# Kernel tuning notes

Hardware: AMD Instinct MI355X
Metric: run time of the kernel (lower is better)

## Reference

```python
import jax, jax.numpy as jnp
import numpy as np

J_THR = 0.5
E_THR = 0.5
STRIDE = 4.0
N_LAYERS = 3
NFEAT = 256
SCORER_HIDDEN = 128


def setup_inputs() -> dict:
    key = jax.random.key(0)
    ks = jax.random.split(key, 8)
    B, C, h, w = 4, NFEAT, 128, 128
    inp = {
        "j_logits": jax.random.normal(ks[0], (B, 1, h, w), dtype=jnp.float32),
        "offsets": jax.random.uniform(ks[1], (B, 2, h, w), dtype=jnp.float32),
        "node_feats_map": jax.random.normal(ks[2], (B, C, h, w), dtype=jnp.float32) * 0.1,
        "W_self": jax.random.normal(ks[3], (N_LAYERS, C, C), dtype=jnp.float32) / np.sqrt(C).astype(np.float32),
        "W_nbr": jax.random.normal(ks[4], (N_LAYERS, C, C), dtype=jnp.float32) / np.sqrt(C).astype(np.float32),
        "b_gnn": jnp.zeros((N_LAYERS, C), dtype=jnp.float32),
        "Ws1": jax.random.normal(ks[5], (2 * C, SCORER_HIDDEN), dtype=jnp.float32) / np.sqrt(2.0 * C).astype(np.float32),
        "bs1": jnp.zeros((SCORER_HIDDEN,), dtype=jnp.float32),
        "Ws2": jax.random.normal(ks[6], (SCORER_HIDDEN,), dtype=jnp.float32) / np.sqrt(SCORER_HIDDEN).astype(np.float32),
        "bs2": jnp.zeros((), dtype=jnp.float32),
        "max_nodes": 256,
    }
    return inp


def _complete_graph(n):
    # src repeats node i (n-1) times; dst enumerates all j != i, matching torch complete_graph
    src = np.repeat(np.arange(n), n - 1)
    grid = np.tile(np.arange(n), (n, 1))
    dst = grid[~np.eye(n, dtype=bool)]
    return jnp.asarray(src, dtype=jnp.int32), jnp.asarray(dst, dtype=jnp.int32)


def reference(j_logits, offsets, node_feats_map, W_self, W_nbr, b_gnn, Ws1, bs1, Ws2, bs2, max_nodes):
    B, _, h, w = j_logits.shape
    C = node_feats_map.shape[1]
    N = int(max_nodes)
    src, dst = _complete_graph(N)  # [E], E = N*(N-1)

    def per_image(jl, off, nmap):
        prob = jax.nn.sigmoid(jl[0].reshape(-1))            # [h*w]
        topv, topi = jax.lax.top_k(prob, N)                  # fixed-size stream compaction
        valid = topv > J_THR                                 # [N] mask replacing dynamic nonzero
        iy = topi // w
        ix = topi % w
        yo = off[0].reshape(-1)[topi]
        xo = off[1].reshape(-1)[topi]
        xs = (ix.astype(jnp.float32) + 0.5 + xo) * STRIDE
        ys = (iy.astype(jnp.float32) + 0.5 + yo) * STRIDE
        nodes = jnp.stack([xs, ys], axis=-1)                 # [N,2]
        x = nmap.reshape(C, -1)[:, topi].T * valid[:, None].astype(nmap.dtype)  # [N,C]
        ev = (valid[src] & valid[dst]).astype(x.dtype)       # [E] edge validity
        deg = jax.ops.segment_sum(ev, dst, num_segments=N)   # [N]
        inv_deg = jnp.where(deg > 0, 1.0 / jnp.maximum(deg, 1.0), 0.0)
        for l in range(W_self.shape[0]):
            msg = x[src] * ev[:, None]                       # gather + mask [E,C]
            agg = jax.ops.segment_sum(msg, dst, num_segments=N) * inv_deg[:, None]
            x = jax.nn.relu(x @ W_self[l] + agg @ W_nbr[l] + b_gnn[l]) * valid[:, None].astype(x.dtype)
        hcat = jnp.concatenate([x[src], x[dst]], axis=-1)    # [E,2C]
        hid = jax.nn.relu(hcat @ Ws1 + bs1)                  # [E,H]
        logits = hid @ Ws2 + bs2                             # [E]
        probs = jax.nn.sigmoid(logits)
        keep = (probs > E_THR) & (ev > 0)
        return nodes, x, logits, keep

    nodes, node_emb, edge_logits, keep = jax.vmap(per_image)(j_logits, offsets, node_feats_map)
    return nodes, node_emb, edge_logits, keep
```

## Files before the change

kernel.cpp:

```cpp
#include <hip/hip_runtime.h>

#define NPIX 16384
#define NN   256
#define CC   256
#define HH   128
#define EE   65280
#define BB   4
#define NG   32

typedef __attribute__((ext_vector_type(8))) short short8;
typedef __attribute__((ext_vector_type(4))) float f32x4;

__device__ __forceinline__ unsigned short f2bf(float f){
  unsigned b = __float_as_uint(f);
  return (unsigned short)((b + 0x7fffu + ((b >> 16) & 1u)) >> 16);
}
__device__ __forceinline__ float bf2f(unsigned short s){ return __uint_as_float(((unsigned)s) << 16); }
__device__ __forceinline__ float bf_lo(unsigned u){ return __uint_as_float(u << 16); }
__device__ __forceinline__ float bf_hi(unsigned u){ return __uint_as_float(u & 0xFFFF0000u); }

__global__ __launch_bounds__(1024) void k_topk(
    const float* __restrict__ jl, const float* __restrict__ off,
    int* __restrict__ topi, int* __restrict__ valid, float* __restrict__ inv_deg,
    float* __restrict__ out_nodes, float* __restrict__ Sbuf,
    const float* __restrict__ Wself, const float* __restrict__ Wnbr,
    const float* __restrict__ Ws1,
    unsigned short* __restrict__ wbfT, unsigned short* __restrict__ wuvT)
{
  __shared__ int hist[NG][257];
  __shared__ int histT[256];
  __shared__ unsigned long long s_sel[NN];
  __shared__ unsigned long long s_T;
  __shared__ int s_digit, s_krem, s_cnt, s_vcnt, s_break;
  __shared__ float tile[32][33];

  const int bid = blockIdx.x;
  const int tid = threadIdx.x;

  if (bid >= BB) {
    const int blk = bid - BB;
    const int m = blk >> 6;
    const int t = blk & 63;
    const int r  = tid >> 5;
    const int cl = tid & 31;
    if (m < 6) {
      const int tr = t >> 3, tc = t & 7;
      const float* src = (m < 3) ? (Wself + (size_t)m*65536) : (Wnbr + (size_t)(m-3)*65536);
      tile[r][cl] = src[(size_t)(tr*32 + r)*256 + tc*32 + cl];
      __syncthreads();
      wbfT[(size_t)m*65536 + (size_t)(tc*32 + r)*256 + tr*32 + cl] = f2bf(tile[cl][r]);
    } else {
      const int tr = t >> 2, tc = t & 3;
      tile[r][cl] = Ws1[(size_t)(tr*32 + r)*128 + tc*32 + cl];
      __syncthreads();
      int h  = tc*32 + r;
      int cgx = tr*32 + cl;
      int col = h + ((cgx >= 256) ? 128 : 0);
      wuvT[(size_t)col*256 + (cgx & 255)] = f2bf(tile[cl][r]);
    }
    return;
  }

  const int b = bid;
  const int grp = tid >> 5;
  if (tid == 0) { s_cnt = 0; s_vcnt = 0; }

  {
    int l = tid >> 8, c = tid & 255;
    Sbuf[l*BB*CC + b*CC + c] = 0.0f;
  }

  unsigned long long rk[16];
  const float* p = jl + (size_t)b * NPIX;
  #pragma unroll
  for (int r = 0; r < 16; ++r) {
    int i = tid + (r << 10);
    float x = p[i];
    float pr = 1.0f / (1.0f + expf(-x));
    unsigned bits = __float_as_uint(pr);
    rk[r] = ((unsigned long long)bits << 32) | (unsigned)(0xFFFFFFFFu - (unsigned)i);
  }

  unsigned long long prefix = 0;
  int k = NN;
  int shift = 56;
  int brk = 0;
  for (int pass = 0; pass < 8 && !brk; ++pass) {
    shift = 56 - 8 * pass;
    for (int i = tid; i < NG * 257; i += 1024) ((int*)hist)[i] = 0;
    __syncthreads();
    unsigned long long pmask = (pass == 0) ? 0ULL : (~0ULL << (shift + 8));
    #pragma unroll
    for (int r = 0; r < 16; ++r) {
      unsigned long long kk = rk[r];
      if ((kk & pmask) == prefix)
        atomicAdd(&hist[grp][(int)((kk >> shift) & 255)], 1);
    }
    __syncthreads();
    if (tid < 256) {
      int t = 0;
      #pragma unroll
      for (int g = 0; g < NG; ++g) t += hist[g][tid];
      histT[tid] = t;
    }
    __syncthreads();
    if (tid < 64) {
      int h0 = histT[4*tid + 0], h1 = histT[4*tid + 1];
      int h2 = histT[4*tid + 2], h3 = histT[4*tid + 3];
      int tot = h0 + h1 + h2 + h3;
      int suf = tot;
      #pragma unroll
      for (int d = 1; d < 64; d <<= 1) {
        int o = __shfl_down(suf, d);
        if (tid + d < 64) suf += o;
      }
      int above = suf - tot;
      int c3 = h3 + above;
      int c2 = c3 + h2;
      int c1 = c2 + h1;
      int c0 = c1 + h0;
      if      (c3 >= k && above < k) { s_digit = 4*tid+3; s_krem = k - above; s_break = (h3 == 1); }
      else if (c2 >= k && c3    < k) { s_digit = 4*tid+2; s_krem = k - c3;    s_break = (h2 == 1); }
      else if (c1 >= k && c2    < k) { s_digit = 4*tid+1; s_krem = k - c2;    s_break = (h1 == 1); }
      else if (c0 >= k && c1    < k) { s_digit = 4*tid+0; s_krem = k - c1;    s_break = (h0 == 1); }
    }
    __syncthreads();
    prefix |= ((unsigned long long)s_digit) << shift;
    k = s_krem;
    brk = s_break;
  }

  if (shift == 0) {
    if (tid == 0) s_T = prefix;
  } else {
    unsigned long long known_mask = ~0ULL << shift;
    #pragma unroll
    for (int r = 0; r < 16; ++r)
      if ((rk[r] & known_mask) == prefix) s_T = rk[r];
  }
  __syncthreads();
  unsigned long long T = s_T;

  #pragma unroll
  for (int r = 0; r < 16; ++r) {
    unsigned long long kk = rk[r];
    if (kk >= T) { int pos = atomicAdd(&s_cnt, 1); s_sel[pos] = kk; }
  }
  __syncthreads();

  int my_rank = -1, my_v = 0;
  if (tid < NN) {
    unsigned long long mine = s_sel[tid];
    int rank = 0;
    #pragma unroll 16
    for (int j = 0; j < NN; ++j) rank += (s_sel[j] > mine) ? 1 : 0;
    unsigned bits = (unsigned)(mine >> 32);
    int v = bits > 0x3F000000u ? 1 : 0;
    int idx = (int)(0xFFFFFFFFu - (unsigned)(mine & 0xFFFFFFFFull));
    if (v) atomicAdd(&s_vcnt, 1);
    topi[b*NN + rank] = idx;
    valid[b*NN + rank] = v;
    int iy = idx >> 7;
    int ix = idx & 127;
    float yo = off[((size_t)b*2 + 0) * NPIX + idx];
    float xo = off[((size_t)b*2 + 1) * NPIX + idx];
    out_nodes[(b*NN + rank)*2 + 0] = ((float)ix + 0.5f + xo) * 4.0f;
    out_nodes[(b*NN + rank)*2 + 1] = ((float)iy + 0.5f + yo) * 4.0f;
    my_rank = rank; my_v = v;
  }
  __syncthreads();
  if (tid < NN) {
    int V = s_vcnt;
    inv_deg[b*NN + my_rank] = (my_v && V >= 2) ? 1.0f / (float)(V - 1) : 0.0f;
  }
}

__global__ __launch_bounds__(256) void k_gather(
    const float* __restrict__ nmap, const int* __restrict__ topi,
    const int* __restrict__ valid, unsigned short* __restrict__ x, float* __restrict__ S0)
{
  __shared__ int s_pix[8], s_val[8];
  const int blk = blockIdx.x;
  const int b  = blk >> 5;
  const int n0 = (blk & 31) * 8;
  const int c = threadIdx.x;
  if (c < 8) { s_pix[c] = topi[b*NN + n0 + c]; s_val[c] = valid[b*NN + n0 + c]; }
  __syncthreads();
  const float* base = nmap + ((size_t)b*CC + c) * NPIX;
  float sum = 0.f;
  #pragma unroll
  for (int r = 0; r < 8; ++r) {
    float val = s_val[r] ? base[s_pix[r]] : 0.0f;
    unsigned short hb = f2bf(val);
    x[(size_t)(b*NN + n0 + r)*CC + c] = hb;
    sum += bf2f(hb);
  }
  if (sum != 0.0f) atomicAdd(&S0[b*CC + c], sum);
}

__global__ __launch_bounds__(256) void k_gnn(
    const unsigned short* __restrict__ x, const float* __restrict__ S,
    const float* __restrict__ inv_deg, const int* __restrict__ valid,
    const unsigned short* __restrict__ wT1, const unsigned short* __restrict__ wT2,
    const float* __restrict__ bias, unsigned short* __restrict__ xout,
    float* __restrict__ Snext,
    float* __restrict__ out_emb)
{
  __shared__ float sA1[16][33];
  __shared__ float sA2[16][33];
  __shared__ float sP2p[8][33];
  __shared__ float sP2[32];
  const int mt = blockIdx.x >> 3;
  const int cg = blockIdx.x & 7;
  const int row0 = mt * 16;
  const int b = row0 >> 8;
  const int tid = threadIdx.x;
  const int wave = tid >> 6;
  const int lane = tid & 63;

  {
    const int cl = tid >> 3;
    const int kw = tid & 7;
    const uint4*  w4 = (const uint4*)(wT2 + (size_t)(cg*32 + cl)*256 + kw*32);
    const float4* S4 = (const float4*)(S + b*CC + kw*32);
    float a = 0.f;
    #pragma unroll
    for (int i = 0; i < 4; ++i) {
      uint4 q = w4[i];
      float4 s0 = S4[2*i], s1 = S4[2*i + 1];
      a += s0.x*bf_lo(q.x) + s0.y*bf_hi(q.x) + s0.z*bf_lo(q.y) + s0.w*bf_hi(q.y);
      a += s1.x*bf_lo(q.z) + s1.y*bf_hi(q.z) + s1.z*bf_lo(q.w) + s1.w*bf_hi(q.w);
    }
    sP2p[kw][cl] = a;
  }
  __syncthreads();
  if (tid < 32) {
    float s = 0.f;
    #pragma unroll
    for (int g = 0; g < 8; ++g) s += sP2p[g][tid];
    sP2[tid] = s;
  }

  const unsigned short* wT = (wave < 2) ? wT1 : wT2;
  const int colbase = cg*32 + (wave & 1)*16;
  const int arow = row0 + (lane & 15);
  const int koff = (lane >> 4) * 8;

  const short8* aptr = (const short8*)(x + (size_t)arow*256 + koff);
  const short8* bptr = (const short8*)(wT + (size_t)(colbase + (lane & 15))*256 + koff);

  f32x4 acc = {0.f, 0.f, 0.f, 0.f};
  #pragma unroll
  for (int kk = 0; kk < 8; ++kk) {
    short8 af = aptr[kk*4];
    short8 bf = bptr[kk*4];
    acc = __builtin_amdgcn_mfma_f32_16x16x32_bf16(af, bf, acc, 0, 0, 0);
  }

  {
    float* dst = (wave < 2) ? &sA1[0][0] : &sA2[0][0];
    int ccol = (wave & 1)*16 + (lane & 15);
    #pragma unroll
    for (int r = 0; r < 4; ++r) {
      int crow = (lane >> 4)*4 + r;
      dst[crow*33 + ccol] = acc[r];
    }
  }
  __syncthreads();

  const int row = tid >> 4;
  const int cp2 = tid & 15;
  const int gr = row0 + row;
  const int c0 = cg*32 + 2*cp2;
  float inv = inv_deg[gr];
  int   va  = valid[gr];
  float a10 = sA1[row][2*cp2], a11 = sA1[row][2*cp2+1];
  float a20 = sA2[row][2*cp2], a21 = sA2[row][2*cp2+1];
  float p0 = sP2[2*cp2], p1 = sP2[2*cp2+1];
  float o0 = fmaxf(a10 + inv*(p0 - a20) + bias[c0],     0.f); o0 = va ? o0 : 0.f;
  float o1 = fmaxf(a11 + inv*(p1 - a21) + bias[c0 + 1], 0.f); o1 = va ? o1 : 0.f;

  unsigned short h0 = f2bf(o0), h1 = f2bf(o1);
  ((unsigned*)xout)[(size_t)gr*128 + (cg*16 + cp2)] = (unsigned)h0 | ((unsigned)h1 << 16);
  if (out_emb) {
    float2 v; v.x = o0; v.y = o1;
    *(float2*)&out_emb[(size_t)gr*CC + c0] = v;
  }
  if (Snext) {
    __syncthreads();
    sA1[row][2*cp2]   = bf2f(h0);
    sA1[row][2*cp2+1] = bf2f(h1);
    __syncthreads();
    if (tid < 32) {
      float s = 0.f;
      #pragma unroll
      for (int r = 0; r < 16; ++r) s += sA1[r][tid];
      if (s != 0.f) atomicAdd(&Snext[b*CC + cg*32 + tid], s);
    }
  }
}

__global__ __launch_bounds__(256) void k_uv(
    const unsigned short* __restrict__ x, const unsigned short* __restrict__ wuvT,
    const float* __restrict__ bs1,
    float* __restrict__ u, float* __restrict__ vt)
{
  const int mt = blockIdx.x >> 2;
  const int cg = blockIdx.x & 3;
  const int row0 = mt * 16;
  const int b = row0 >> 8;
  const int wave = threadIdx.x >> 6;
  const int lane = threadIdx.x & 63;
  const int col = cg*64 + wave*16 + (lane & 15);
  const int arow = row0 + (lane & 15);
  const int koff = (lane >> 4) * 8;
  const short8* aptr = (const short8*)(x + (size_t)arow*256 + koff);
  const short8* bptr = (const short8*)(wuvT + (size_t)col*256 + koff);
  f32x4 acc = {0.f, 0.f, 0.f, 0.f};
  #pragma unroll
  for (int kk = 0; kk < 8; ++kk)
    acc = __builtin_amdgcn_mfma_f32_16x16x32_bf16(aptr[kk*4], bptr[kk*4], acc, 0, 0, 0);
  const int rbase = row0 + (lane >> 4)*4;
  if (col < HH) {
    float bv = bs1[col];
    #pragma unroll
    for (int r = 0; r < 4; ++r)
      u[(size_t)(rbase + r)*HH + col] = acc[r] + bv;
  } else {
    float4 v; v.x = acc[0]; v.y = acc[1]; v.z = acc[2]; v.w = acc[3];
    *(float4*)&vt[(size_t)(b*HH + (col - HH))*NN + rbase] = v;
  }
}

__global__ __launch_bounds__(256) void k_edges(
    const float* __restrict__ u, const float* __restrict__ vt,
    const float* __restrict__ Ws2, const float* __restrict__ bs2,
    const int* __restrict__ valid,
    float* __restrict__ out_logits, float* __restrict__ out_keep)
{
  __shared__ float su[4][HH];
  __shared__ float sws[HH];
  __shared__ float4 red[3][4][64];
  const int b  = blockIdx.x >> 6;
  const int ig = blockIdx.x & 63;
  const int i0 = ig * 4;
  const int tid = threadIdx.x;
  const int jq = tid & 63;
  const int kh = tid >> 6;

  #pragma unroll
  for (int r = 0; r < 2; ++r) {
    int idx = tid + 256*r;
    int il = idx >> 7, h = idx & 127;
    su[il][h] = u[((size_t)(b*NN + i0 + il))*HH + h];
  }
  if (tid < HH) sws[tid] = Ws2[tid];
  __syncthreads();

  const float4* vbase = (const float4*)(vt + (size_t)(b*HH + kh*32)*NN) + jq;
  float4 acc0 = {0,0,0,0}, acc1 = {0,0,0,0}, acc2 = {0,0,0,0}, acc3 = {0,0,0,0};
  #pragma unroll 4
  for (int h = 0; h < 32; ++h) {
    float4 v = vbase[(size_t)h*64];
    float wh = sws[kh*32 + h];
    float u0 = su[0][kh*32 + h];
    float u1 = su[1][kh*32 + h];
    float u2 = su[2][kh*32 + h];
    float u3 = su[3][kh*32 + h];
    acc0.x += fmaxf(u0 + v.x, 0.f)*wh; acc0.y += fmaxf(u0 + v.y, 0.f)*wh;
    acc0.z += fmaxf(u0 + v.z, 0.f)*wh; acc0.w += fmaxf(u0 + v.w, 0.f)*wh;
    acc1.x += fmaxf(u1 + v.x, 0.f)*wh; acc1.y += fmaxf(u1 + v.y, 0.f)*wh;
    acc1.z += fmaxf(u1 + v.z, 0.f)*wh; acc1.w += fmaxf(u1 + v.w, 0.f)*wh;
    acc2.x += fmaxf(u2 + v.x, 0.f)*wh; acc2.y += fmaxf(u2 + v.y, 0.f)*wh;
    acc2.z += fmaxf(u2 + v.z, 0.f)*wh; acc2.w += fmaxf(u2 + v.w, 0.f)*wh;
    acc3.x += fmaxf(u3 + v.x, 0.f)*wh; acc3.y += fmaxf(u3 + v.y, 0.f)*wh;
    acc3.z += fmaxf(u3 + v.z, 0.f)*wh; acc3.w += fmaxf(u3 + v.w, 0.f)*wh;
  }
  if (kh > 0) {
    red[kh-1][0][jq] = acc0;
    red[kh-1][1][jq] = acc1;
    red[kh-1][2][jq] = acc2;
    red[kh-1][3][jq] = acc3;
  }
  __syncthreads();
  if (kh == 0) {
    float bs = bs2[0];
    float* Lb = out_logits + (size_t)b*EE;
    float* Kb = out_keep   + (size_t)b*EE;
    int j0 = 4*jq;
    int vj0 = valid[b*NN + j0 + 0];
    int vj1 = valid[b*NN + j0 + 1];
    int vj2 = valid[b*NN + j0 + 2];
    int vj3 = valid[b*NN + j0 + 3];
    #pragma unroll
    for (int il = 0; il < 4; ++il) {
      int i = i0 + il;
      int vi = valid[b*NN + i];
      float4 a = (il == 0) ? acc0 : (il == 1) ? acc1 : (il == 2) ? acc2 : acc3;
      float4 r0 = red[0][il][jq], r1 = red[1][il][jq], r2 = red[2][il][jq];
      float lg0 = a.x + r0.x + r1.x + r2.x + bs;
      float lg1 = a.y + r0.y + r1.y + r2.y + bs;
      float lg2 = a.z + r0.z + r1.z + r2.z + bs;
      float lg3 = a.w + r0.w + r1.w + r2.w + bs;
      {
        int j = j0;
        if (j != i) { int e = i*255 + (j < i ? j : j-1);
          Lb[e] = lg0; Kb[e] = (lg0 > 0.f && vi && vj0) ? 1.0f : 0.0f; }
      }
      {
        int j = j0 + 1;
        if (j != i) { int e = i*255 + (j < i ? j : j-1);
          Lb[e] = lg1; Kb[e] = (lg1 > 0.f && vi && vj1) ? 1.0f : 0.0f; }
      }
      {
        int j = j0 + 2;
        if (j != i) { int e = i*255 + (j < i ? j : j-1);
          Lb[e] = lg2; Kb[e] = (lg2 > 0.f && vi && vj2) ? 1.0f : 0.0f; }
      }
      {
        int j = j0 + 3;
        if (j != i) { int e = i*255 + (j < i ? j : j-1);
          Lb[e] = lg3; Kb[e] = (lg3 > 0.f && vi && vj3) ? 1.0f : 0.0f; }
      }
    }
  }
}

extern "C" void kernel_launch(void* const* d_in, const int* in_sizes, int n_in,
                              void* d_out, int out_size, void* d_ws, size_t ws_size,
                              hipStream_t stream) {
  const float* jl    = (const float*)d_in[0];
  const float* off   = (const float*)d_in[1];
  const float* nmap  = (const float*)d_in[2];
  const float* Wself = (const float*)d_in[3];
  const float* Wnbr  = (const float*)d_in[4];
  const float* bg    = (const float*)d_in[5];
  const float* Ws1   = (const float*)d_in[6];
  const float* bs1   = (const float*)d_in[7];
  const float* Ws2   = (const float*)d_in[8];
  const float* bs2   = (const float*)d_in[9];

  char* ws = (char*)d_ws;
  int*   topi    = (int*)  (ws + 0);
  int*   valid   = (int*)  (ws + 4096);
  float* inv_deg = (float*)(ws + 8192);
  float* Sbuf    = (float*)(ws + 12288);
  unsigned short* xa = (unsigned short*)(ws + 28672);
  unsigned short* xb = (unsigned short*)(ws + 552960);
  float* u       = (float*)(ws + 1077248);
  float* vt      = (float*)(ws + 1601536);
  unsigned short* wbfT = (unsigned short*)(ws + 2125824);
  unsigned short* wuvT = (unsigned short*)(ws + 2912256);

  float* out        = (float*)d_out;
  float* out_nodes  = out;
  float* out_emb    = out + 2048;
  float* out_logits = out + 264192;
  float* out_keep   = out + 525312;

  hipLaunchKernelGGL(k_topk,   dim3(BB + 448), dim3(1024), 0, stream,
                     jl, off, topi, valid, inv_deg, out_nodes, Sbuf,
                     Wself, Wnbr, Ws1, wbfT, wuvT);
  hipLaunchKernelGGL(k_gather, dim3(BB*32),    dim3(256),  0, stream,
                     nmap, topi, valid, xa, Sbuf);

  unsigned short* xc = xa; unsigned short* xn = xb;
  for (int l = 0; l < 3; ++l) {
    hipLaunchKernelGGL(k_gnn, dim3(512), dim3(256),  0, stream,
                       xc, Sbuf + l*BB*CC, inv_deg, valid,
                       wbfT + (size_t)l*65536, wbfT + (size_t)(3 + l)*65536, bg + l*CC,
                       xn,
                       (l < 2) ? (Sbuf + (l+1)*BB*CC) : (float*)nullptr,
                       (l == 2) ? out_emb : (float*)nullptr);
    unsigned short* t = xc; xc = xn; xn = t;
  }

  hipLaunchKernelGGL(k_uv,    dim3(256),   dim3(256), 0, stream, xc, wuvT, bs1, u, vt);
  hipLaunchKernelGGL(k_edges, dim3(BB*64), dim3(256), 0, stream,
                     u, vt, Ws2, bs2, valid, out_logits, out_keep);
}
```

Before: 72.43 us.

## Fuse last GNN layer with edge-scorer U/V projection into one kernel

```diff
diff --git a/kernel.cpp b/kernel.cpp
--- a/kernel.cpp
+++ b/kernel.cpp
@@ -203,8 +203,7 @@
     const float* __restrict__ inv_deg, const int* __restrict__ valid,
     const unsigned short* __restrict__ wT1, const unsigned short* __restrict__ wT2,
     const float* __restrict__ bias, unsigned short* __restrict__ xout,
-    float* __restrict__ Snext,
-    float* __restrict__ out_emb)
+    float* __restrict__ Snext)
 {
   __shared__ float sA1[16][33];
   __shared__ float sA2[16][33];
@@ -251,11 +250,8 @@
 
   f32x4 acc = {0.f, 0.f, 0.f, 0.f};
   #pragma unroll
-  for (int kk = 0; kk < 8; ++kk) {
-    short8 af = aptr[kk*4];
-    short8 bf = bptr[kk*4];
-    acc = __builtin_amdgcn_mfma_f32_16x16x32_bf16(af, bf, acc, 0, 0, 0);
-  }
+  for (int kk = 0; kk < 8; ++kk)
+    acc = __builtin_amdgcn_mfma_f32_16x16x32_bf16(aptr[kk*4], bptr[kk*4], acc, 0, 0, 0);
 
   {
     float* dst = (wave < 2) ? &sA1[0][0] : &sA2[0][0];
@@ -282,11 +278,7 @@
 
   unsigned short h0 = f2bf(o0), h1 = f2bf(o1);
   ((unsigned*)xout)[(size_t)gr*128 + (cg*16 + cp2)] = (unsigned)h0 | ((unsigned)h1 << 16);
-  if (out_emb) {
-    float2 v; v.x = o0; v.y = o1;
-    *(float2*)&out_emb[(size_t)gr*CC + c0] = v;
-  }
-  if (Snext) {
+  {
     __syncthreads();
     sA1[row][2*cp2]   = bf2f(h0);
     sA1[row][2*cp2+1] = bf2f(h1);
@@ -300,35 +292,103 @@
   }
 }
 
-__global__ __launch_bounds__(256) void k_uv(
-    const unsigned short* __restrict__ x, const unsigned short* __restrict__ wuvT,
-    const float* __restrict__ bs1,
-    float* __restrict__ u, float* __restrict__ vt)
+__global__ __launch_bounds__(256) void k_gnn_uv(
+    const unsigned short* __restrict__ x, const float* __restrict__ S,
+    const float* __restrict__ inv_deg, const int* __restrict__ valid,
+    const unsigned short* __restrict__ wT1, const unsigned short* __restrict__ wT2,
+    const float* __restrict__ bias,
+    const unsigned short* __restrict__ wuvT, const float* __restrict__ bs1,
+    float* __restrict__ u, float* __restrict__ vt,
+    float* __restrict__ out_emb)
 {
-  const int mt = blockIdx.x >> 2;
-  const int cg = blockIdx.x & 3;
-  const int row0 = mt * 16;
+  __shared__ float sA1[16][33];
+  __shared__ float sA2[16][33];
+  __shared__ float sP2[256];
+  __shared__ unsigned short xtile[16][264];
+  const int row0 = blockIdx.x * 16;
   const int b = row0 >> 8;
-  const int wave = threadIdx.x >> 6;
-  const int lane = threadIdx.x & 63;
-  const int col = cg*64 + wave*16 + (lane & 15);
+  const int tid = threadIdx.x;
+  const int wave = tid >> 6;
+  const int lane = tid & 63;
+
+  {
+    const uint4*  w4 = (const uint4*)(wT2 + (size_t)tid*256);
+    const float4* S4 = (const float4*)(S + b*CC);
+    float a = 0.f;
+    #pragma unroll 8
+    for (int i = 0; i < 32; ++i) {
+      uint4 q = w4[i];
+      float4 s0 = S4[2*i], s1 = S4[2*i + 1];
+      a += s0.x*bf_lo(q.x) + s0.y*bf_hi(q.x) + s0.z*bf_lo(q.y) + s0.w*bf_hi(q.y);
+      a += s1.x*bf_lo(q.z) + s1.y*bf_hi(q.z) + s1.z*bf_lo(q.w) + s1.w*bf_hi(q.w);
+    }
+    sP2[tid] = a;
+  }
+
   const int arow = row0 + (lane & 15);
   const int koff = (lane >> 4) * 8;
   const short8* aptr = (const short8*)(x + (size_t)arow*256 + koff);
-  const short8* bptr = (const short8*)(wuvT + (size_t)col*256 + koff);
-  f32x4 acc = {0.f, 0.f, 0.f, 0.f};
+  const unsigned short* wT = (wave < 2) ? wT1 : wT2;
+  const int row = tid >> 4;
+  const int cp2 = tid & 15;
+  const int gr = row0 + row;
+  const float inv = inv_deg[gr];
+  const int   va  = valid[gr];
+
+  for (int cg = 0; cg < 8; ++cg) {
+    const int colbase = cg*32 + (wave & 1)*16;
+    const short8* bptr = (const short8*)(wT + (size_t)(colbase + (lane & 15))*256 + koff);
+    f32x4 acc = {0.f, 0.f, 0.f, 0.f};
+    #pragma unroll
+    for (int kk = 0; kk < 8; ++kk)
+      acc = __builtin_amdgcn_mfma_f32_16x16x32_bf16(aptr[kk*4], bptr[kk*4], acc, 0, 0, 0);
+    {
+      float* dst = (wave < 2) ? &sA1[0][0] : &sA2[0][0];
+      int ccol = (wave & 1)*16 + (lane & 15);
+      #pragma unroll
+      for (int r = 0; r < 4; ++r) {
+        int crow = (lane >> 4)*4 + r;
+        dst[crow*33 + ccol] = acc[r];
+      }
+    }
+    __syncthreads();
+    {
+      const int c0 = cg*32 + 2*cp2;
+      float a10 = sA1[row][2*cp2], a11 = sA1[row][2*cp2+1];
+      float a20 = sA2[row][2*cp2], a21 = sA2[row][2*cp2+1];
+      float p0 = sP2[c0], p1 = sP2[c0 + 1];
+      float o0 = fmaxf(a10 + inv*(p0 - a20) + bias[c0],     0.f); o0 = va ? o0 : 0.f;
+      float o1 = fmaxf(a11 + inv*(p1 - a21) + bias[c0 + 1], 0.f); o1 = va ? o1 : 0.f;
+      unsigned short h0 = f2bf(o0), h1 = f2bf(o1);
+      xtile[row][c0]     = h0;
+      xtile[row][c0 + 1] = h1;
+      float2 v; v.x = o0; v.y = o1;
+      *(float2*)&out_emb[(size_t)gr*CC + c0] = v;
+    }
+    __syncthreads();
+  }
+
+  const int lrow = lane & 15;
   #pragma unroll
-  for (int kk = 0; kk < 8; ++kk)
-    acc = __builtin_amdgcn_mfma_f32_16x16x32_bf16(aptr[kk*4], bptr[kk*4], acc, 0, 0, 0);
-  const int rbase = row0 + (lane >> 4)*4;
-  if (col < HH) {
-    float bv = bs1[col];
-    #pragma unroll
-    for (int r = 0; r < 4; ++r)
-      u[(size_t)(rbase + r)*HH + col] = acc[r] + bv;
-  } else {
-    float4 v; v.x = acc[0]; v.y = acc[1]; v.z = acc[2]; v.w = acc[3];
-    *(float4*)&vt[(size_t)(b*HH + (col - HH))*NN + rbase] = v;
+  for (int ct = 0; ct < 4; ++ct) {
+    const int col = ct*64 + wave*16 + lrow;
+    const short8* bptr = (const short8*)(wuvT + (size_t)col*256 + koff);
+    f32x4 acc = {0.f, 0.f, 0.f, 0.f};
+    #pragma unroll
+    for (int kk = 0; kk < 8; ++kk) {
+      short8 af = *(const short8*)&xtile[lrow][koff + kk*32];
+      acc = __builtin_amdgcn_mfma_f32_16x16x32_bf16(af, bptr[kk*4], acc, 0, 0, 0);
+    }
+    const int rbase = row0 + (lane >> 4)*4;
+    if (col < HH) {
+      float bv = bs1[col];
+      #pragma unroll
+      for (int r = 0; r < 4; ++r)
+        u[(size_t)(rbase + r)*HH + col] = acc[r] + bv;
+    } else {
+      float4 v; v.x = acc[0]; v.y = acc[1]; v.z = acc[2]; v.w = acc[3];
+      *(float4*)&vt[(size_t)(b*HH + (col - HH))*NN + rbase] = v;
+    }
   }
 }
 
@@ -465,17 +525,19 @@
                      nmap, topi, valid, xa, Sbuf);
 
   unsigned short* xc = xa; unsigned short* xn = xb;
-  for (int l = 0; l < 3; ++l) {
+  for (int l = 0; l < 2; ++l) {
     hipLaunchKernelGGL(k_gnn, dim3(512), dim3(256),  0, stream,
                        xc, Sbuf + l*BB*CC, inv_deg, valid,
                        wbfT + (size_t)l*65536, wbfT + (size_t)(3 + l)*65536, bg + l*CC,
-                       xn,
-                       (l < 2) ? (Sbuf + (l+1)*BB*CC) : (float*)nullptr,
-                       (l == 2) ? out_emb : (float*)nullptr);
+                       xn, Sbuf + (l+1)*BB*CC);
     unsigned short* t = xc; xc = xn; xn = t;
   }
 
-  hipLaunchKernelGGL(k_uv,    dim3(256),   dim3(256), 0, stream, xc, wuvT, bs1, u, vt);
+  hipLaunchKernelGGL(k_gnn_uv, dim3(64), dim3(256), 0, stream,
+                     xc, Sbuf + 2*BB*CC, inv_deg, valid,
+                     wbfT + (size_t)2*65536, wbfT + (size_t)5*65536, bg + 2*CC,
+                     wuvT, bs1, u, vt, out_emb);
+
   hipLaunchKernelGGL(k_edges, dim3(BB*64), dim3(256), 0, stream,
                      u, vt, Ws2, bs2, valid, out_logits, out_keep);
 }
```

New measurement: 86.06 us. +18.8%, slower.
